# Performance work log

Measured on AMD Instinct MI355X. Metric: run time of the kernel, lower is better.

## Reference

```python
import jax, jax.numpy as jnp
import numpy as np

D = 1024      # embedding_dimension
F = 4096      # intermediate_dimension
E = 8         # num_experts
K = 2         # top_k
B, S = 4, 2048


def setup_inputs() -> dict:
    key = jax.random.key(0)
    ks = jax.random.split(key, 6)
    scale_in = 1.0 / np.sqrt(D)
    scale_mid = 1.0 / np.sqrt(F)
    return {
        "x": jax.random.normal(ks[0], (B, S, D), dtype=jnp.float32),
        "router_w": jax.random.normal(ks[1], (E, D), dtype=jnp.float32) * scale_in,   # nn.Linear weight [out,in]
        "w1": jax.random.normal(ks[2], (E, F, D), dtype=jnp.float32) * scale_in,
        "b1": jax.random.normal(ks[3], (E, F), dtype=jnp.float32) * 0.01,
        "w2": jax.random.normal(ks[4], (E, D, F), dtype=jnp.float32) * scale_mid,
        "b2": jax.random.normal(ks[5], (E, D), dtype=jnp.float32) * 0.01,
    }


def reference(x, router_w, w1, b1, w2, b2):
    orig_shape = x.shape
    xf = x.reshape(-1, D)                                  # [T, D]
    logits = jnp.einsum("td,ed->te", xf, router_w)        # [T, E]
    top_vals, top_idx = jax.lax.top_k(logits, K)           # [T, K]
    probs = jax.nn.softmax(top_vals, axis=-1)              # [T, K]

    out = jnp.zeros_like(xf)
    for e in range(E):  # small fixed expert loop; masked dense combine
        # combine weight per token for expert e (0 if not routed)
        w = jnp.sum(jnp.where(top_idx == e, probs, 0.0), axis=-1)   # [T]
        h = jax.nn.gelu(jnp.einsum("td,fd->tf", xf, w1[e]) + b1[e], approximate=False)
        y = jnp.einsum("tf,df->td", h, w2[e]) + b2[e]
        out = out + w[:, None] * y
    return out.reshape(orig_shape)
```

## Files before the change

kernel.cpp:

```cpp
#include <hip/hip_runtime.h>
#include <hip/hip_bf16.h>
#include <stdint.h>

#define D 1024
#define F 4096
#define E 8
#define T 8192
#define SLOT_CAP 17408
#define BM 128
#define BK 32
#define EP_STRIDE 136

typedef __attribute__((ext_vector_type(8))) short bf16x8;
typedef __attribute__((ext_vector_type(4))) float f32x4;
typedef __attribute__((ext_vector_type(8))) unsigned short u16x8;

__device__ __forceinline__ unsigned short f2bf(float f) {
  unsigned u = __float_as_uint(f);
  u += 0x7fffu + ((u >> 16) & 1u);
  return (unsigned short)(u >> 16);
}
__device__ __forceinline__ float bf2f(unsigned short u) {
  return __uint_as_float(((unsigned)u) << 16);
}

__device__ __forceinline__ float gelu_f(float v) {
  float s = fabsf(v) * 0.70710678118654752f;
  float t = __builtin_amdgcn_rcpf(fmaf(0.3275911f, s, 1.0f));
  float p = fmaf(t, 1.061405429f, -1.453152027f);
  p = fmaf(t, p, 1.421413741f);
  p = fmaf(t, p, -0.284496736f);
  p = fmaf(t, p, 0.254829592f);
  p = p * t;
  float e = 1.0f - p * __expf(-s * s);
  e = copysignf(e, v);
  return 0.5f * v * (1.0f + e);
}

__device__ __forceinline__ void gload16(const void* g, void* l) {
  auto gp = (const __attribute__((address_space(1))) unsigned int*)(uintptr_t)g;
  auto lp = (__attribute__((address_space(3))) unsigned int*)(unsigned)(uintptr_t)l;
  __builtin_amdgcn_global_load_lds(gp, lp, 16, 0, 0);
}

__global__ __launch_bounds__(256) void prep_kernel(const float* __restrict__ x,
                                                   const float* __restrict__ rw,
                                                   const float* __restrict__ w1,
                                                   const float* __restrict__ w2,
                                                   int* __restrict__ tok_e,
                                                   float* __restrict__ tok_p,
                                                   unsigned short* __restrict__ xg,
                                                   unsigned short* __restrict__ w1g,
                                                   unsigned short* __restrict__ w2g) {
  if (blockIdx.x >= 2048) {
    const int n8 = E * F * D / 8;
    int i = (blockIdx.x - 2048) * 256 + threadIdx.x;
    const float* in = w1;
    unsigned short* out = w1g;
    if (i >= n8) { i -= n8; in = w2; out = w2g; }
    const float4* p = (const float4*)in + (size_t)i * 2;
    float4 a = p[0], b = p[1];
    u16x8 o;
    o[0] = f2bf(a.x); o[1] = f2bf(a.y); o[2] = f2bf(a.z); o[3] = f2bf(a.w);
    o[4] = f2bf(b.x); o[5] = f2bf(b.y); o[6] = f2bf(b.z); o[7] = f2bf(b.w);
    *(u16x8*)(out + (size_t)i * 8) = o;
    return;
  }
  int t = blockIdx.x * 4 + (threadIdx.x >> 6);
  int lane = threadIdx.x & 63;
  const float* xp = x + (size_t)t * D;
  unsigned short* xgp = xg + (size_t)t * D;
  double acc[E];
#pragma unroll
  for (int e = 0; e < E; e++) acc[e] = 0.0;
  for (int j = 0; j < D / 64; j++) {
    float xv = xp[j * 64 + lane];
    xgp[j * 64 + lane] = f2bf(xv);
#pragma unroll
    for (int e = 0; e < E; e++) acc[e] += (double)xv * (double)rw[e * D + j * 64 + lane];
  }
#pragma unroll
  for (int e = 0; e < E; e++) {
#pragma unroll
    for (int off = 32; off >= 1; off >>= 1) acc[e] += __shfl_xor(acc[e], off, 64);
  }
  if (lane == 0) {
    double v0 = -1e300, v1 = -1e300;
    int i0 = 0, i1 = 0;
#pragma unroll
    for (int e = 0; e < E; e++) {
      double v = acc[e];
      if (v > v0) { v1 = v0; i1 = i0; v0 = v; i0 = e; }
      else if (v > v1) { v1 = v; i1 = e; }
    }
    double e1 = exp(v1 - v0);
    double s = 1.0 + e1;
    tok_e[2 * t] = i0; tok_e[2 * t + 1] = i1;
    tok_p[2 * t] = (float)(1.0 / s);
    tok_p[2 * t + 1] = (float)(e1 / s);
  }
}

__global__ __launch_bounds__(64) void bucket_kernel(const int* __restrict__ tok_e,
                                                    int* __restrict__ perm,
                                                    int* __restrict__ slot_of,
                                                    int* __restrict__ counts,
                                                    int* __restrict__ offp) {
  const int e = blockIdx.x;
  const int lane = threadIdx.x;
  int cnt[E];
#pragma unroll
  for (int ee = 0; ee < E; ee++) cnt[ee] = 0;
  for (int idx = lane; idx < 2 * T; idx += 64) {
    int v = tok_e[idx];
#pragma unroll
    for (int ee = 0; ee < E; ee++) cnt[ee] += (v == ee) ? 1 : 0;
  }
#pragma unroll
  for (int ee = 0; ee < E; ee++) {
#pragma unroll
    for (int off = 32; off >= 1; off >>= 1) cnt[ee] += __shfl_xor(cnt[ee], off, 64);
  }
  int off_e[E + 1];
  int o = 0;
#pragma unroll
  for (int ee = 0; ee < E; ee++) { off_e[ee] = o; o += (cnt[ee] + (BM - 1)) & ~(BM - 1); }
  off_e[E] = o;
  if (e == 0 && lane == 0) {
#pragma unroll
    for (int ee = 0; ee < E; ee++) { counts[ee] = cnt[ee]; offp[ee] = off_e[ee]; }
    offp[E] = o;
  }
  int base = 0, mycnt = 0, myend = 0;
#pragma unroll
  for (int ee = 0; ee < E; ee++) {
    if (ee == e) { base = off_e[ee]; mycnt = cnt[ee]; myend = off_e[ee + 1]; }
  }
  const int pad0 = base + mycnt;
  for (int r = 0; r < 2 * T / 64; r++) {
    int idx = r * 64 + lane;
    int v = tok_e[idx];
    bool m = (v == e);
    unsigned long long mask = __ballot(m);
    int pre = __popcll(mask & ((1ull << lane) - 1ull));
    if (m) {
      int slot = base + pre;
      perm[slot] = idx >> 1;
      slot_of[idx] = slot;
    }
    base += __popcll(mask);
  }
  for (int i = pad0 + lane; i < myend; i += 64) perm[i] = 0;
}

__global__ __launch_bounds__(256, 3) void gemm1_kernel(const unsigned short* __restrict__ xg,
                                                       const unsigned short* __restrict__ w1g,
                                                       const float* __restrict__ b1,
                                                       const int* __restrict__ perm,
                                                       const int* __restrict__ offp,
                                                       const int* __restrict__ counts,
                                                       unsigned short* __restrict__ hbuf) {
  const int id = blockIdx.x;
  const int xcd = id & 7, loc = id >> 3;
  const int q = loc / 136, r = loc % 136;
  const int bm = xcd * 17 + (r >> 3);
  const int bn = q * 8 + (r & 7);
  const int row0 = bm * BM;
  if (row0 >= offp[E]) return;
  int e = 0;
#pragma unroll
  for (int i = 0; i < E; i++) if (row0 >= offp[i + 1]) e = i + 1;
  if (row0 >= offp[e] + counts[e]) return;

  const int tid = threadIdx.x, lane = tid & 63, w = tid >> 6;
  __shared__ __align__(16) unsigned short smem[BM * EP_STRIDE];
  unsigned short* As0 = smem;
  unsigned short* Bs0 = smem + 8192;

  const unsigned short* gsrc[4];
  unsigned short* ldst[4];
#pragma unroll
  for (int i = 0; i < 4; i++) {
    int ch = tid + 256 * i;
    if (ch < 512) {
      int ar = ch >> 2, ac = (ch & 3) * 8;
      gsrc[i] = xg + (size_t)perm[row0 + ar] * D + ac;
      ldst[i] = As0 + ch * 8;
    } else {
      int c = ch - 512;
      int br = c >> 2, bc = (c & 3) * 8;
      gsrc[i] = w1g + ((size_t)e * F + (size_t)bn * BM + br) * D + bc;
      ldst[i] = Bs0 + c * 8;
    }
  }
  auto stage = [&](int k0, int buf) {
#pragma unroll
    for (int i = 0; i < 4; i++) gload16(gsrc[i] + k0, ldst[i] + buf * (BM * BK));
  };

  f32x4 acc[4][4] = {};
  const int wr = (w >> 1) * 64, wc = (w & 1) * 64;
  const int fr = lane & 15, fq = lane >> 4;

  stage(0, 0);
  __syncthreads();
  int cur = 0;
  for (int k0 = 0; k0 < D; k0 += BK) {
    if (k0 + BK < D) stage(k0 + BK, cur ^ 1);
    bf16x8 a[4], b[4];
#pragma unroll
    for (int m = 0; m < 4; m++) a[m] = *(const bf16x8*)&As0[cur * 4096 + (wr + m * 16 + fr) * BK + fq * 8];
#pragma unroll
    for (int n = 0; n < 4; n++) b[n] = *(const bf16x8*)&Bs0[cur * 4096 + (wc + n * 16 + fr) * BK + fq * 8];
#pragma unroll
    for (int m = 0; m < 4; m++)
#pragma unroll
      for (int n = 0; n < 4; n++)
        acc[m][n] = __builtin_amdgcn_mfma_f32_16x16x32_bf16(a[m], b[n], acc[m][n], 0, 0, 0);
    __syncthreads();
    cur ^= 1;
  }

#pragma unroll
  for (int n = 0; n < 4; n++) {
    int cl = wc + n * 16 + fr;
    float bias = b1[e * F + bn * BM + cl];
#pragma unroll
    for (int m = 0; m < 4; m++) {
#pragma unroll
      for (int j = 0; j < 4; j++) {
        int rl = wr + m * 16 + fq * 4 + j;
        smem[rl * EP_STRIDE + cl] = f2bf(gelu_f(acc[m][n][j] + bias));
      }
    }
  }
  __syncthreads();
#pragma unroll
  for (int i = 0; i < 8; i++) {
    int idx = tid + i * 256;
    int r2 = idx >> 4, c = (idx & 15) * 8;
    u16x8 v = *(const u16x8*)&smem[r2 * EP_STRIDE + c];
    *(u16x8*)&hbuf[(size_t)(row0 + r2) * F + bn * BM + c] = v;
  }
}

__global__ __launch_bounds__(256, 3) void gemm2_kernel(const unsigned short* __restrict__ hbuf,
                                                       const unsigned short* __restrict__ w2g,
                                                       const float* __restrict__ b2,
                                                       const int* __restrict__ offp,
                                                       const int* __restrict__ counts,
                                                       unsigned short* __restrict__ ypart) {
  const int id = blockIdx.x;
  const int swz = (id & 7) * 272 + (id >> 3);
  const int bn = swz & 7;
  const int ks = (swz >> 3) & 1;
  const int bm = swz >> 4;
  const int row0 = bm * BM;
  if (row0 >= offp[E]) return;
  int e = 0;
#pragma unroll
  for (int i = 0; i < E; i++) if (row0 >= offp[i + 1]) e = i + 1;
  const int valid_end = offp[e] + counts[e];
  if (row0 >= valid_end) return;

  const int tid = threadIdx.x, lane = tid & 63, w = tid >> 6;
  __shared__ __align__(16) unsigned short smem[BM * EP_STRIDE];
  unsigned short* As0 = smem;
  unsigned short* Bs0 = smem + 8192;

  const int kbase = ks * (F / 2);
  const unsigned short* gsrc[4];
  unsigned short* ldst[4];
#pragma unroll
  for (int i = 0; i < 4; i++) {
    int ch = tid + 256 * i;
    if (ch < 512) {
      int ar = ch >> 2, ac = (ch & 3) * 8;
      gsrc[i] = hbuf + (size_t)(row0 + ar) * F + kbase + ac;
      ldst[i] = As0 + ch * 8;
    } else {
      int c = ch - 512;
      int br = c >> 2, bc = (c & 3) * 8;
      gsrc[i] = w2g + ((size_t)e * D + (size_t)bn * BM + br) * F + kbase + bc;
      ldst[i] = Bs0 + c * 8;
    }
  }
  auto stage = [&](int k0, int buf) {
#pragma unroll
    for (int i = 0; i < 4; i++) gload16(gsrc[i] + k0, ldst[i] + buf * (BM * BK));
  };

  f32x4 acc[4][4] = {};
  const int wr = (w >> 1) * 64, wc = (w & 1) * 64;
  const int fr = lane & 15, fq = lane >> 4;

  stage(0, 0);
  __syncthreads();
  int cur = 0;
  for (int k0 = 0; k0 < F / 2; k0 += BK) {
    if (k0 + BK < F / 2) stage(k0 + BK, cur ^ 1);
    bf16x8 a[4], b[4];
#pragma unroll
    for (int m = 0; m < 4; m++) a[m] = *(const bf16x8*)&As0[cur * 4096 + (wr + m * 16 + fr) * BK + fq * 8];
#pragma unroll
    for (int n = 0; n < 4; n++) b[n] = *(const bf16x8*)&Bs0[cur * 4096 + (wc + n * 16 + fr) * BK + fq * 8];
#pragma unroll
    for (int m = 0; m < 4; m++)
#pragma unroll
      for (int n = 0; n < 4; n++)
        acc[m][n] = __builtin_amdgcn_mfma_f32_16x16x32_bf16(a[m], b[n], acc[m][n], 0, 0, 0);
    __syncthreads();
    cur ^= 1;
  }

#pragma unroll
  for (int n = 0; n < 4; n++) {
    int cl = wc + n * 16 + fr;
    float bias = (ks == 0) ? b2[e * D + bn * BM + cl] : 0.0f;
#pragma unroll
    for (int m = 0; m < 4; m++) {
#pragma unroll
      for (int j = 0; j < 4; j++) {
        int rl = wr + m * 16 + fq * 4 + j;
        smem[rl * EP_STRIDE + cl] = f2bf(acc[m][n][j] + bias);
      }
    }
  }
  __syncthreads();
  unsigned short* ybase = ypart + (size_t)ks * SLOT_CAP * D;
#pragma unroll
  for (int i = 0; i < 8; i++) {
    int idx = tid + i * 256;
    int r2 = idx >> 4, c = (idx & 15) * 8;
    if (row0 + r2 < valid_end) {
      u16x8 v = *(const u16x8*)&smem[r2 * EP_STRIDE + c];
      *(u16x8*)&ybase[(size_t)(row0 + r2) * D + bn * BM + c] = v;
    }
  }
}

__global__ __launch_bounds__(256) void combine_kernel(const unsigned short* __restrict__ ypart,
                                                      const int* __restrict__ slot_of,
                                                      const float* __restrict__ tok_p,
                                                      float* __restrict__ out) {
  int i = blockIdx.x * 256 + threadIdx.x;
  int t = i >> 7;
  int g8 = i & 127;
  int s0 = slot_of[2 * t], s1 = slot_of[2 * t + 1];
  float g0 = tok_p[2 * t], g1 = tok_p[2 * t + 1];
  const unsigned short* p0 = ypart;
  const unsigned short* p1 = ypart + (size_t)SLOT_CAP * D;
  u16x8 a0 = *(const u16x8*)(p0 + (size_t)s0 * D + g8 * 8);
  u16x8 b0 = *(const u16x8*)(p1 + (size_t)s0 * D + g8 * 8);
  u16x8 a1 = *(const u16x8*)(p0 + (size_t)s1 * D + g8 * 8);
  u16x8 b1 = *(const u16x8*)(p1 + (size_t)s1 * D + g8 * 8);
  float o[8];
#pragma unroll
  for (int j = 0; j < 8; j++)
    o[j] = g0 * (bf2f(a0[j]) + bf2f(b0[j])) + g1 * (bf2f(a1[j]) + bf2f(b1[j]));
  float4* op = (float4*)(out + (size_t)t * D + g8 * 8);
  op[0] = make_float4(o[0], o[1], o[2], o[3]);
  op[1] = make_float4(o[4], o[5], o[6], o[7]);
}

extern "C" void kernel_launch(void* const* d_in, const int* in_sizes, int n_in,
                              void* d_out, int out_size, void* d_ws, size_t ws_size,
                              hipStream_t stream) {
  const float* x = (const float*)d_in[0];
  const float* rw = (const float*)d_in[1];
  const float* w1 = (const float*)d_in[2];
  const float* b1 = (const float*)d_in[3];
  const float* w2 = (const float*)d_in[4];
  const float* b2 = (const float*)d_in[5];
  float* out = (float*)d_out;

  char* ws = (char*)d_ws;
  size_t off = 0;
  auto alloc = [&](size_t bytes) {
    void* p = ws + off;
    off = (off + bytes + 255) & ~(size_t)255;
    return p;
  };
  int* counts = (int*)alloc(E * 4);
  int* offp = (int*)alloc((E + 1) * 4);
  int* tok_e = (int*)alloc((size_t)T * 2 * 4);
  float* tok_p = (float*)alloc((size_t)T * 2 * 4);
  int* perm = (int*)alloc((size_t)SLOT_CAP * 4);
  int* slot_of = (int*)alloc((size_t)T * 2 * 4);
  unsigned short* xg = (unsigned short*)alloc((size_t)T * D * 2);
  unsigned short* w1g = (unsigned short*)alloc((size_t)E * F * D * 2);
  unsigned short* w2g = (unsigned short*)alloc((size_t)E * D * F * 2);
  unsigned short* hbuf = (unsigned short*)alloc((size_t)SLOT_CAP * F * 2);
  unsigned short* ypart = xg;
  (void)ws_size; (void)in_sizes; (void)n_in; (void)out_size;

  hipLaunchKernelGGL(prep_kernel, dim3(2048 + 2 * E * F * D / 8 / 256), dim3(256), 0, stream,
                     x, rw, w1, w2, tok_e, tok_p, xg, w1g, w2g);
  hipLaunchKernelGGL(bucket_kernel, dim3(E), dim3(64), 0, stream,
                     tok_e, perm, slot_of, counts, offp);
  hipLaunchKernelGGL(gemm1_kernel, dim3(4352), dim3(256), 0, stream,
                     xg, w1g, b1, perm, offp, counts, hbuf);
  hipLaunchKernelGGL(gemm2_kernel, dim3(2176), dim3(256), 0, stream,
                     hbuf, w2g, b2, offp, counts, ypart);
  hipLaunchKernelGGL(combine_kernel, dim3(T * D / 8 / 256), dim3(256), 0, stream,
                     ypart, slot_of, tok_p, out);
}
```

Measured before the change: 587.3 us.

## Rewrite expert GEMM1 with 256x256 tiles, 4-stage pipeline and swizzled LDS

GEMM1 moves from 128x128 tiles with 256 threads and double buffering to 256x256 tiles with 512 threads, a 4-deep async load ring, XOR-swizzled LDS layout, split MFMA phases with setprio, and explicit vmcnt waits. Expert padding is raised to 256 rows (with larger slot capacity and gemm2 grid) to match the new tile size. The intent is more data reuse per tile, better latency hiding and fewer LDS bank conflicts, at the cost of more padded rows and higher register and LDS pressure, which lowers occupancy.

```diff
diff --git a/kernel.cpp b/kernel.cpp
--- a/kernel.cpp
+++ b/kernel.cpp
@@ -6,10 +6,15 @@
 #define F 4096
 #define E 8
 #define T 8192
-#define SLOT_CAP 17408
+#define SLOT_CAP 18432
 #define BM 128
 #define BK 32
 #define EP_STRIDE 136
+
+#define BM2 256
+#define BN2 256
+#define BK2 32
+#define EP2 268
 
 typedef __attribute__((ext_vector_type(8))) short bf16x8;
 typedef __attribute__((ext_vector_type(4))) float f32x4;
@@ -124,7 +129,7 @@
   int off_e[E + 1];
   int o = 0;
 #pragma unroll
-  for (int ee = 0; ee < E; ee++) { off_e[ee] = o; o += (cnt[ee] + (BM - 1)) & ~(BM - 1); }
+  for (int ee = 0; ee < E; ee++) { off_e[ee] = o; o += (cnt[ee] + 255) & ~255; }
   off_e[E] = o;
   if (e == 0 && lane == 0) {
 #pragma unroll
@@ -153,7 +158,7 @@
   for (int i = pad0 + lane; i < myend; i += 64) perm[i] = 0;
 }
 
-__global__ __launch_bounds__(256, 3) void gemm1_kernel(const unsigned short* __restrict__ xg,
+__global__ __launch_bounds__(512, 2) void gemm1_kernel(const unsigned short* __restrict__ xg,
                                                        const unsigned short* __restrict__ w1g,
                                                        const float* __restrict__ b1,
                                                        const int* __restrict__ perm,
@@ -161,86 +166,136 @@
                                                        const int* __restrict__ counts,
                                                        unsigned short* __restrict__ hbuf) {
   const int id = blockIdx.x;
-  const int xcd = id & 7, loc = id >> 3;
-  const int q = loc / 136, r = loc % 136;
-  const int bm = xcd * 17 + (r >> 3);
-  const int bn = q * 8 + (r & 7);
-  const int row0 = bm * BM;
+  const int swz = (id & 7) * 144 + (id >> 3);
+  const int bm = swz >> 4, bn = swz & 15;
+  const int row0 = bm * BM2;
   if (row0 >= offp[E]) return;
   int e = 0;
 #pragma unroll
   for (int i = 0; i < E; i++) if (row0 >= offp[i + 1]) e = i + 1;
   if (row0 >= offp[e] + counts[e]) return;
 
-  const int tid = threadIdx.x, lane = tid & 63, w = tid >> 6;
-  __shared__ __align__(16) unsigned short smem[BM * EP_STRIDE];
-  unsigned short* As0 = smem;
-  unsigned short* Bs0 = smem + 8192;
-
-  const unsigned short* gsrc[4];
-  unsigned short* ldst[4];
-#pragma unroll
-  for (int i = 0; i < 4; i++) {
-    int ch = tid + 256 * i;
-    if (ch < 512) {
-      int ar = ch >> 2, ac = (ch & 3) * 8;
-      gsrc[i] = xg + (size_t)perm[row0 + ar] * D + ac;
-      ldst[i] = As0 + ch * 8;
-    } else {
-      int c = ch - 512;
-      int br = c >> 2, bc = (c & 3) * 8;
-      gsrc[i] = w1g + ((size_t)e * F + (size_t)bn * BM + br) * D + bc;
-      ldst[i] = Bs0 + c * 8;
-    }
-  }
-  auto stage = [&](int k0, int buf) {
-#pragma unroll
-    for (int i = 0; i < 4; i++) gload16(gsrc[i] + k0, ldst[i] + buf * (BM * BK));
+  const int t = threadIdx.x, lane = t & 63, w = t >> 6;
+  const int wm = w >> 2, wn = w & 3;
+  const int fr = lane & 15, fq = lane >> 4;
+
+  __shared__ __align__(16) unsigned short smem[65536];
+
+  const int srow = t >> 2;
+  const int c = (t & 3) ^ (srow & 3);
+  const unsigned short* srcA[2];
+  const unsigned short* srcB[2];
+  {
+    int p0 = perm[row0 + srow], p1 = perm[row0 + 128 + srow];
+    srcA[0] = xg + (size_t)p0 * D + c * 8;
+    srcA[1] = xg + (size_t)p1 * D + c * 8;
+    srcB[0] = w1g + ((size_t)e * F + (size_t)bn * BN2 + srow) * D + c * 8;
+    srcB[1] = w1g + ((size_t)e * F + (size_t)bn * BN2 + 128 + srow) * D + c * 8;
+  }
+
+  float biasv[4];
+#pragma unroll
+  for (int n = 0; n < 4; n++) {
+    biasv[n] = b1[e * F + bn * BN2 + wn * 64 + n * 16 + fr];
+    asm volatile("" :: "v"(biasv[n]));
+  }
+
+  auto stageA = [&](int tk) {
+    unsigned short* base = smem + (tk & 3) * 16384 + t * 8;
+    gload16(srcA[0] + tk * 32, base);
+    gload16(srcA[1] + tk * 32, base + 4096);
   };
-
-  f32x4 acc[4][4] = {};
-  const int wr = (w >> 1) * 64, wc = (w & 1) * 64;
-  const int fr = lane & 15, fq = lane >> 4;
-
-  stage(0, 0);
+  auto stageB = [&](int tk) {
+    unsigned short* base = smem + (tk & 3) * 16384 + 8192 + t * 8;
+    gload16(srcB[0] + tk * 32, base);
+    gload16(srcB[1] + tk * 32, base + 4096);
+  };
+
+  int aoff[8], boff[4];
+#pragma unroll
+  for (int m = 0; m < 8; m++) {
+    int row = wm * 128 + m * 16 + fr;
+    aoff[m] = row * 32 + ((fq ^ (row & 3)) * 8);
+  }
+#pragma unroll
+  for (int n = 0; n < 4; n++) {
+    int row = wn * 64 + n * 16 + fr;
+    boff[n] = 8192 + row * 32 + ((fq ^ (row & 3)) * 8);
+  }
+
+  f32x4 acc[8][4] = {};
+
+  stageA(0); stageB(0);
+  stageA(1); stageB(1);
+  stageA(2); stageB(2);
+  asm volatile("s_waitcnt vmcnt(8)" ::: "memory");
+  __builtin_amdgcn_s_barrier();
+  __builtin_amdgcn_sched_barrier(0);
+
+  const int NK = D / BK2;
+#pragma unroll 4
+  for (int kt = 0; kt < NK; ++kt) {
+    const unsigned short* tb = smem + (kt & 3) * 16384;
+    bf16x8 a0[4], b[4];
+#pragma unroll
+    for (int m = 0; m < 4; m++) a0[m] = *(const bf16x8*)(tb + aoff[m]);
+#pragma unroll
+    for (int n = 0; n < 4; n++) b[n] = *(const bf16x8*)(tb + boff[n]);
+    if (kt + 3 < NK) stageA(kt + 3);
+    __builtin_amdgcn_s_setprio(1);
+#pragma unroll
+    for (int m = 0; m < 4; m++)
+#pragma unroll
+      for (int n = 0; n < 4; n++)
+        acc[m][n] = __builtin_amdgcn_mfma_f32_16x16x32_bf16(a0[m], b[n], acc[m][n], 0, 0, 0);
+    __builtin_amdgcn_s_setprio(0);
+    __builtin_amdgcn_s_barrier();
+    __builtin_amdgcn_sched_barrier(0);
+    bf16x8 a1[4];
+#pragma unroll
+    for (int m = 0; m < 4; m++) a1[m] = *(const bf16x8*)(tb + aoff[4 + m]);
+    if (kt + 3 < NK) stageB(kt + 3);
+    __builtin_amdgcn_s_setprio(1);
+#pragma unroll
+    for (int m = 0; m < 4; m++)
+#pragma unroll
+      for (int n = 0; n < 4; n++)
+        acc[4 + m][n] = __builtin_amdgcn_mfma_f32_16x16x32_bf16(a1[m], b[n], acc[4 + m][n], 0, 0, 0);
+    __builtin_amdgcn_s_setprio(0);
+    if (kt < NK - 3)       { asm volatile("s_waitcnt vmcnt(8)" ::: "memory"); }
+    else if (kt == NK - 3) { asm volatile("s_waitcnt vmcnt(4)" ::: "memory"); }
+    else if (kt == NK - 2) { asm volatile("s_waitcnt vmcnt(0)" ::: "memory"); }
+    __builtin_amdgcn_s_barrier();
+    __builtin_amdgcn_sched_barrier(0);
+  }
+
   __syncthreads();
-  int cur = 0;
-  for (int k0 = 0; k0 < D; k0 += BK) {
-    if (k0 + BK < D) stage(k0 + BK, cur ^ 1);
-    bf16x8 a[4], b[4];
-#pragma unroll
-    for (int m = 0; m < 4; m++) a[m] = *(const bf16x8*)&As0[cur * 4096 + (wr + m * 16 + fr) * BK + fq * 8];
-#pragma unroll
-    for (int n = 0; n < 4; n++) b[n] = *(const bf16x8*)&Bs0[cur * 4096 + (wc + n * 16 + fr) * BK + fq * 8];
-#pragma unroll
-    for (int m = 0; m < 4; m++)
-#pragma unroll
-      for (int n = 0; n < 4; n++)
-        acc[m][n] = __builtin_amdgcn_mfma_f32_16x16x32_bf16(a[m], b[n], acc[m][n], 0, 0, 0);
+  unsigned short* ep = smem;
+#pragma unroll
+  for (int p = 0; p < 2; p++) {
+    if (wm == p) {
+#pragma unroll
+      for (int n = 0; n < 4; n++) {
+        int col = wn * 64 + n * 16 + fr;
+#pragma unroll
+        for (int m = 0; m < 8; m++) {
+#pragma unroll
+          for (int j = 0; j < 4; j++) {
+            int lr = m * 16 + fq * 4 + j;
+            ep[lr * EP2 + col] = f2bf(gelu_f(acc[m][n][j] + biasv[n]));
+          }
+        }
+      }
+    }
     __syncthreads();
-    cur ^= 1;
-  }
-
-#pragma unroll
-  for (int n = 0; n < 4; n++) {
-    int cl = wc + n * 16 + fr;
-    float bias = b1[e * F + bn * BM + cl];
-#pragma unroll
-    for (int m = 0; m < 4; m++) {
-#pragma unroll
-      for (int j = 0; j < 4; j++) {
-        int rl = wr + m * 16 + fq * 4 + j;
-        smem[rl * EP_STRIDE + cl] = f2bf(gelu_f(acc[m][n][j] + bias));
-      }
-    }
-  }
-  __syncthreads();
-#pragma unroll
-  for (int i = 0; i < 8; i++) {
-    int idx = tid + i * 256;
-    int r2 = idx >> 4, c = (idx & 15) * 8;
-    u16x8 v = *(const u16x8*)&smem[r2 * EP_STRIDE + c];
-    *(u16x8*)&hbuf[(size_t)(row0 + r2) * F + bn * BM + c] = v;
+#pragma unroll
+    for (int i = 0; i < 8; i++) {
+      int idx = t + i * 512;
+      int r2 = idx >> 5, c8 = (idx & 31) * 8;
+      u16x8 v = *(const u16x8*)&ep[r2 * EP2 + c8];
+      *(u16x8*)&hbuf[(size_t)(row0 + p * 128 + r2) * F + (size_t)bn * BN2 + c8] = v;
+    }
+    __syncthreads();
   }
 }
 
@@ -251,7 +306,7 @@
                                                        const int* __restrict__ counts,
                                                        unsigned short* __restrict__ ypart) {
   const int id = blockIdx.x;
-  const int swz = (id & 7) * 272 + (id >> 3);
+  const int swz = (id & 7) * 288 + (id >> 3);
   const int bn = swz & 7;
   const int ks = (swz >> 3) & 1;
   const int bm = swz >> 4;
@@ -398,9 +453,9 @@
                      x, rw, w1, w2, tok_e, tok_p, xg, w1g, w2g);
   hipLaunchKernelGGL(bucket_kernel, dim3(E), dim3(64), 0, stream,
                      tok_e, perm, slot_of, counts, offp);
-  hipLaunchKernelGGL(gemm1_kernel, dim3(4352), dim3(256), 0, stream,
+  hipLaunchKernelGGL(gemm1_kernel, dim3(1152), dim3(512), 0, stream,
                      xg, w1g, b1, perm, offp, counts, hbuf);
-  hipLaunchKernelGGL(gemm2_kernel, dim3(2176), dim3(256), 0, stream,
+  hipLaunchKernelGGL(gemm2_kernel, dim3(2304), dim3(256), 0, stream,
                      hbuf, w2g, b2, offp, counts, ypart);
   hipLaunchKernelGGL(combine_kernel, dim3(T * D / 8 / 256), dim3(256), 0, stream,
                      ypart, slot_of, tok_p, out);
```

Result: slower. 626.8 us (+6.7%).
